# Kernel tuning notes

Hardware: AMD Instinct MI355X
Metric: run time of the kernel (lower is better)

The kernel has to match this reference:

```python
import jax, jax.numpy as jnp
import numpy as np
import math

HIDDEN = 1024
HEADS = 16
HEAD_DIM = HIDDEN // HEADS


def setup_inputs() -> dict:
    key = jax.random.key(0)
    ks = jax.random.split(key, 9)
    s = 1.0 / math.sqrt(HIDDEN)
    return {
        "x": jax.random.normal(ks[0], (4, 2048, HIDDEN), dtype=jnp.float32),
        "Wq": jax.random.normal(ks[1], (HIDDEN, HIDDEN), dtype=jnp.float32) * s,
        "bq": jnp.zeros((HIDDEN,), dtype=jnp.float32),
        "Wk": jax.random.normal(ks[2], (HIDDEN, HIDDEN), dtype=jnp.float32) * s,
        "bk": jnp.zeros((HIDDEN,), dtype=jnp.float32),
        "Wv": jax.random.normal(ks[3], (HIDDEN, HIDDEN), dtype=jnp.float32) * s,
        "bv": jnp.zeros((HIDDEN,), dtype=jnp.float32),
        "Wo": jax.random.normal(ks[4], (HIDDEN, HIDDEN), dtype=jnp.float32) * s,
        "bo": jnp.zeros((HIDDEN,), dtype=jnp.float32),
    }


def reference(x, Wq, bq, Wk, bk, Wv, bv, Wo, bo):
    B, L, D = x.shape
    H, hd = HEADS, HEAD_DIM
    # QKV projections (weights stored as [in, out], i.e. torch W.T)
    q = (x @ Wq + bq).reshape(B, L, H, hd).transpose(0, 2, 1, 3)  # [B,H,L,hd]
    k = (x @ Wk + bk).reshape(B, L, H, hd).transpose(0, 2, 1, 3)
    v = (x @ Wv + bv).reshape(B, L, H, hd).transpose(0, 2, 1, 3)
    scores = jnp.einsum("bhqd,bhkd->bhqk", q, k) / math.sqrt(hd)  # [B,H,L,L]
    causal_mask = jnp.triu(jnp.full((L, L), -jnp.inf, dtype=scores.dtype), k=1)
    att = jax.nn.softmax(scores + causal_mask, axis=-1)
    out = jnp.einsum("bhqk,bhkd->bhqd", att, v)  # [B,H,L,hd]
    out = out.transpose(0, 2, 1, 3).reshape(B, L, D)
    return out @ Wo + bo
```

## Files before the change

### kernel.cpp

```cpp
#include <hip/hip_runtime.h>
#include <stdint.h>

#define LOG2E 1.44269504088896340736f

typedef __attribute__((ext_vector_type(8))) short short8;
typedef __attribute__((ext_vector_type(4))) float float4v;
typedef __attribute__((ext_vector_type(4))) unsigned int uint4v;
typedef __attribute__((ext_vector_type(2))) unsigned int uint2v;

typedef const __attribute__((address_space(1))) unsigned int gu32;
typedef __attribute__((address_space(3))) unsigned int lu32;

__device__ __forceinline__ void async16(const unsigned short* g, unsigned short* l){
  __builtin_amdgcn_global_load_lds((gu32*)g, (lu32*)l, 16, 0, 0);
}

__device__ __forceinline__ unsigned short f2bf(float f){
  union { float f; unsigned int u; } v; v.f = f;
  unsigned int u = v.u;
  return (unsigned short)((u + 0x7FFFu + ((u >> 16) & 1u)) >> 16);
}
__device__ __forceinline__ unsigned int pkbf(float a, float b){
  unsigned int r;
  asm("v_cvt_pk_bf16_f32 %0, %1, %2" : "=v"(r) : "v"(a), "v"(b));
  return r;
}

__device__ __forceinline__ void pl32(unsigned int &a, unsigned int &b){
#if __has_builtin(__builtin_amdgcn_permlane32_swap)
  uint2v r = __builtin_amdgcn_permlane32_swap(a, b, false, false);
  a = r[0]; b = r[1];
#else
  asm("v_permlane32_swap_b32 %0, %1" : "+v"(a), "+v"(b));
#endif
}
__device__ __forceinline__ void pl16(unsigned int &a, unsigned int &b){
#if __has_builtin(__builtin_amdgcn_permlane16_swap)
  uint2v r = __builtin_amdgcn_permlane16_swap(a, b, false, false);
  a = r[0]; b = r[1];
#else
  asm("v_permlane16_swap_b32 %0, %1" : "+v"(a), "+v"(b));
#endif
}

__global__ void prelude_kernel(const float* __restrict__ x, unsigned short* __restrict__ xb,
                               const float* __restrict__ Wq, const float* __restrict__ Wk,
                               const float* __restrict__ Wv, const float* __restrict__ Wo,
                               unsigned short* __restrict__ wqkvT, unsigned short* __restrict__ woT){
  __shared__ float tileS[64][68];
  const int bid = blockIdx.x;
  if (bid < 4096){
    int t = bid * 256 + threadIdx.x;
    const float4v* xp = (const float4v*)x;
    float4v a = xp[2*t], b = xp[2*t+1];
    short8 o;
    o[0]=(short)f2bf(a[0]); o[1]=(short)f2bf(a[1]); o[2]=(short)f2bf(a[2]); o[3]=(short)f2bf(a[3]);
    o[4]=(short)f2bf(b[0]); o[5]=(short)f2bf(b[1]); o[6]=(short)f2bf(b[2]); o[7]=(short)f2bf(b[3]);
    ((short8*)xb)[t] = o;
    return;
  }
  const int wid = bid - 4096;
  int mat = wid >> 8, tile = wid & 255;
  int tk = tile >> 4, tn = tile & 15;
  const float* W = (mat==0)?Wq:(mat==1)?Wk:(mat==2)?Wv:Wo;
  int k0 = tk*64, n0 = tn*64;
  int tid = threadIdx.x;
  #pragma unroll
  for (int it=0; it<4; ++it){
    int idx = tid + it*256;
    int r = idx >> 4, c4 = idx & 15;
    float4v v = *(const float4v*)&W[(uint64_t)(k0+r)*1024 + n0 + c4*4];
    tileS[r][c4*4+0]=v[0]; tileS[r][c4*4+1]=v[1]; tileS[r][c4*4+2]=v[2]; tileS[r][c4*4+3]=v[3];
  }
  __syncthreads();
  unsigned short* dst; int nbase;
  if (mat<3){ dst = wqkvT; nbase = mat*1024 + n0; } else { dst = woT; nbase = n0; }
  #pragma unroll
  for (int it=0; it<2; ++it){
    int idx = tid + it*256;
    int n = idx >> 3, g = idx & 7;
    short8 o;
    #pragma unroll
    for (int j=0;j<8;++j) o[j] = (short)f2bf(tileS[g*8+j][n]);
    *(short8*)&dst[(uint64_t)(nbase+n)*1024 + k0 + g*8] = o;
  }
}

template<int EPI>
__global__ __launch_bounds__(256, 2) void gemm_kernel(
    const unsigned short* __restrict__ A, const unsigned short* __restrict__ BT,
    const float* __restrict__ bias0, const float* __restrict__ bias1, const float* __restrict__ bias2,
    unsigned short* __restrict__ oq, unsigned short* __restrict__ ok,
    unsigned short* __restrict__ ov, float* __restrict__ of)
{
  __shared__ __attribute__((aligned(16))) unsigned short lS[2*128*64];
  unsigned short* lA = lS;
  unsigned short* lB = lS + 128*64;
  const int tid = threadIdx.x, lane = tid & 63, wave = tid >> 6;
  const int wr = wave >> 1, wc = wave & 1;
  const int by = blockIdx.x & 63, bx = blockIdx.x >> 6;
  const int m0 = by * 128, n0 = bx * 128;
  const int c = lane & 15, quad = lane >> 4;
  const float QSCALE = 0.125f * LOG2E;

  float4v acc[4][4];
  #pragma unroll
  for (int i=0;i<4;++i)
    #pragma unroll
    for (int j=0;j<4;++j) acc[i][j] = (float4v){0.f,0.f,0.f,0.f};

  for (int kt = 0; kt < 16; ++kt){
    __syncthreads();
    #pragma unroll
    for (int it=0; it<4; ++it){
      int gl = (wave*4+it)*64 + lane;
      int row = gl >> 3, gp = gl & 7, gs = gp ^ (row & 7);
      async16(&A[(uint64_t)(m0+row)*1024 + kt*64 + gs*8], &lA[gl*8]);
    }
    #pragma unroll
    for (int it=0; it<4; ++it){
      int gl = (wave*4+it)*64 + lane;
      int row = gl >> 3, gp = gl & 7, gs = gp ^ (row & 7);
      async16(&BT[(uint64_t)(n0+row)*1024 + kt*64 + gs*8], &lB[gl*8]);
    }
    __syncthreads();
    #pragma unroll
    for (int kk=0; kk<2; ++kk){
      short8 af[4], bf[4];
      #pragma unroll
      for (int i=0;i<4;++i){
        int row = wr*64 + i*16 + c;
        int g = (quad + kk*4) ^ (row & 7);
        af[i] = *(const short8*)&lA[row*64 + g*8];
      }
      #pragma unroll
      for (int j=0;j<4;++j){
        int row = wc*64 + j*16 + c;
        int g = (quad + kk*4) ^ (row & 7);
        bf[j] = *(const short8*)&lB[row*64 + g*8];
      }
      #pragma unroll
      for (int i=0;i<4;++i)
        #pragma unroll
        for (int j=0;j<4;++j)
          acc[i][j] = __builtin_amdgcn_mfma_f32_16x16x32_bf16(af[i], bf[j], acc[i][j], 0, 0, 0);
    }
  }

  if (EPI == 0){
    const int sel = bx >> 3;
    const int n0l = n0 & 1023;
    const int h0 = n0l >> 6;
    const int bb = m0 >> 11, l0 = m0 & 2047;
    const float* bp = (sel==0)?bias0:(sel==1)?bias1:bias2;
    float bj[4];
    #pragma unroll
    for (int j=0;j<4;++j) bj[j] = bp[n0l + wc*64 + j*16 + c];
    __syncthreads();
    if (sel < 2){
      unsigned short* dst = (sel==0)?oq:ok;
      #pragma unroll
      for (int i=0;i<4;++i){
        #pragma unroll
        for (int r=0;r<4;++r){
          int mloc = wr*64 + i*16 + quad*4 + r;
          #pragma unroll
          for (int j=0;j<4;++j){
            float v = acc[i][j][r] + bj[j];
            if (sel == 0) v *= QSCALE;
            int col = wc*64 + j*16 + c;
            int gg = col >> 3;
            int gs2 = (gg & 8) | ((gg & 7) ^ (mloc & 7));
            lS[mloc*128 + gs2*8 + (col & 7)] = f2bf(v);
          }
        }
      }
      __syncthreads();
      #pragma unroll
      for (int it=0; it<8; ++it){
        int gl = it*256 + tid;
        int row = gl >> 4, gg = gl & 15;
        int gs2 = (gg & 8) | ((gg & 7) ^ (row & 7));
        short8 w = *(const short8*)&lS[row*128 + gs2*8];
        int hh = h0 + (gg >> 3);
        *(short8*)&dst[((uint64_t)(bb*16 + hh)*2048 + l0 + row)*64 + (gg & 7)*8] = w;
      }
    } else {
      #pragma unroll
      for (int i=0;i<4;++i){
        #pragma unroll
        for (int r=0;r<4;++r){
          int mloc = wr*64 + i*16 + quad*4 + r;
          int mgg = mloc >> 3;
          #pragma unroll
          for (int j=0;j<4;++j){
            float v = acc[i][j][r] + bj[j];
            int col = wc*64 + j*16 + c;
            int gsT = (mgg & 8) | ((mgg & 7) ^ (col & 7));
            lS[col*128 + gsT*8 + (mloc & 7)] = f2bf(v);
          }
        }
      }
      __syncthreads();
      #pragma unroll
      for (int it=0; it<8; ++it){
        int idx = it*256 + tid;
        int mg = idx & 15, cc = idx >> 4;
        int gsT2 = (mg & 8) | ((mg & 7) ^ (cc & 7));
        short8 w = *(const short8*)&lS[cc*128 + gsT2*8];
        int hh = h0 + (cc >> 6), d = cc & 63;
        *(short8*)&ov[((uint64_t)(bb*16 + hh)*64 + d)*2048 + l0 + mg*8] = w;
      }
    }
  } else {
    float* lf = (float*)lS;
    float bj[4];
    #pragma unroll
    for (int j=0;j<4;++j) bj[j] = bias0[n0 + wc*64 + j*16 + c];
    #pragma unroll
    for (int half=0; half<2; ++half){
      __syncthreads();
      if (wr == half){
        #pragma unroll
        for (int i=0;i<4;++i){
          #pragma unroll
          for (int r=0;r<4;++r){
            int lrow = i*16 + quad*4 + r;
            #pragma unroll
            for (int j=0;j<4;++j){
              int col = wc*64 + j*16 + c;
              int gg = col >> 2;
              int gs2 = (gg & 24) | ((gg & 7) ^ (lrow & 7));
              lf[lrow*128 + gs2*4 + (col & 3)] = acc[i][j][r] + bj[j];
            }
          }
        }
      }
      __syncthreads();
      #pragma unroll
      for (int it=0; it<8; ++it){
        int gl = it*256 + tid;
        int lrow = gl >> 5, gg = gl & 31;
        int gs2 = (gg & 24) | ((gg & 7) ^ (lrow & 7));
        float4v w = *(const float4v*)&lf[lrow*128 + gs2*4];
        *(float4v*)&of[(uint64_t)(m0 + half*64 + lrow)*1024 + n0 + gg*4] = w;
      }
    }
  }
}

__global__ __launch_bounds__(256, 3) void attn_kernel(
    const unsigned short* __restrict__ q, const unsigned short* __restrict__ k,
    const unsigned short* __restrict__ vt, unsigned short* __restrict__ o)
{
  __shared__ __attribute__((aligned(16))) unsigned short lK[2][64*64];
  __shared__ __attribute__((aligned(16))) unsigned short lV[2][64*64];

  const int idx = blockIdx.x;
  const int bh = idx & 63;
  const int g4 = idx >> 8;
  const int u4 = (idx >> 6) & 3;
  const int qt = (g4==0) ? (15 - u4) : (g4==1) ? (8 + u4) : (g4==2) ? (7 - u4) : u4;
  const int tid = threadIdx.x, lane = tid & 63, wave = tid >> 6;
  const int c = lane & 15, quad = lane >> 4;

  const unsigned short* qh = q  + (uint64_t)bh * (2048*64);
  const unsigned short* kh = k  + (uint64_t)bh * (2048*64);
  const unsigned short* vh = vt + (uint64_t)bh * (64*2048);

  short8 qf[2][2];
  #pragma unroll
  for (int u=0;u<2;++u)
    #pragma unroll
    for (int kk=0;kk<2;++kk){
      int row = qt*128 + u*64 + wave*16 + c;
      qf[u][kk] = *(const short8*)&qh[(uint64_t)row*64 + (kk*4+quad)*8];
    }

  #pragma unroll
  for (int it=0; it<2; ++it){
    int gl = (wave*2+it)*64 + lane;
    int row = gl >> 3, gp = gl & 7, gs = gp ^ (row & 7);
    async16(&kh[(uint64_t)row*64 + gs*8], &lK[0][gl*8]);
    async16(&vh[(uint64_t)row*2048 + gs*8], &lV[0][gl*8]);
  }

  const float4v z4 = {0.f,0.f,0.f,0.f};
  const uint4v onesu = {0x3F803F80u,0x3F803F80u,0x3F803F80u,0x3F803F80u};
  const short8 ones8 = __builtin_bit_cast(short8, onesu);

  float4v accO[2][4];
  #pragma unroll
  for (int u=0;u<2;++u)
    #pragma unroll
    for (int t=0;t<4;++t) accO[u][t] = z4;
  float4v accL4[2];
  accL4[0] = z4; accL4[1] = z4;

  const int ktEnd = 2*qt + 1;

  for (int kt = 0; kt <= ktEnd; ++kt){
    __syncthreads();
    const int cb = kt & 1;

    if (kt < ktEnd){
      const int nb = 1 - cb;
      #pragma unroll
      for (int it=0; it<2; ++it){
        int gl = (wave*2+it)*64 + lane;
        int row = gl >> 3, gp = gl & 7, gs = gp ^ (row & 7);
        async16(&kh[(uint64_t)((kt+1)*64 + row)*64 + gs*8], &lK[nb][gl*8]);
        async16(&vh[(uint64_t)row*2048 + (kt+1)*64 + gs*8], &lV[nb][gl*8]);
      }
    }

    const bool doU0  = (kt != ktEnd);
    const bool lastT = (kt == ktEnd);
    const bool diag0 = doU0 && (kt == 2*qt);

    float4v s[2][4];
    #pragma unroll
    for (int kk=0; kk<2; ++kk){
      short8 kf[4];
      #pragma unroll
      for (int j=0;j<4;++j){
        if (lastT && j > wave) continue;
        int row = j*16 + c;
        int g = (kk*4 + quad) ^ (row & 7);
        kf[j] = *(const short8*)&lK[cb][row*64 + g*8];
      }
      #pragma unroll
      for (int j=0;j<4;++j){
        if (lastT && j > wave) continue;
        s[1][j] = __builtin_amdgcn_mfma_f32_16x16x32_bf16(kf[j], qf[1][kk],
                    (kk==0)? z4 : s[1][j], 0, 0, 0);
      }
      if (doU0){
        #pragma unroll
        for (int j=0;j<4;++j){
          if (diag0 && j > wave) continue;
          s[0][j] = __builtin_amdgcn_mfma_f32_16x16x32_bf16(kf[j], qf[0][kk],
                      (kk==0)? z4 : s[0][j], 0, 0, 0);
        }
      }
    }

    short8 pa[2][2];
    #pragma unroll
    for (int u=1;u>=0;--u){
      if (u==0 && !doU0) continue;
      const bool isDiagU = (u==1) ? lastT : diag0;
      const int qb_u = qt*128 + u*64 + wave*16;
      const bool needMask = (kt*64 + 63 > qb_u);
      const int qg = qb_u + c;
      unsigned int w[4][2];
      #pragma unroll
      for (int j=0;j<4;++j){
        if (isDiagU && j > wave){ w[j][0]=0u; w[j][1]=0u; continue; }
        float p0,p1,p2,p3;
        {
          float4v sv = s[u][j];
          p0 = __builtin_amdgcn_exp2f(sv[0]);
          p1 = __builtin_amdgcn_exp2f(sv[1]);
          p2 = __builtin_amdgcn_exp2f(sv[2]);
          p3 = __builtin_amdgcn_exp2f(sv[3]);
        }
        if (needMask){
          int keyb = kt*64 + j*16 + quad*4;
          if (keyb + 0 > qg) p0 = 0.f;
          if (keyb + 1 > qg) p1 = 0.f;
          if (keyb + 2 > qg) p2 = 0.f;
          if (keyb + 3 > qg) p3 = 0.f;
        }
        w[j][0] = pkbf(p0,p1);
        w[j][1] = pkbf(p2,p3);
      }
      #pragma unroll
      for (int kk=0;kk<2;++kk){
        if (isDiagU && kk==1 && wave < 2) continue;
        unsigned int a0 = w[2*kk+0][0], b0 = w[2*kk+1][0];
        unsigned int a1 = w[2*kk+0][1], b1 = w[2*kk+1][1];
        pl32(a0,b0); pl32(a1,b1);
        pl16(a0,b0); pl16(a1,b1);
        uint4v uv; uv[0]=a0; uv[1]=a1; uv[2]=b0; uv[3]=b1;
        pa[u][kk] = __builtin_bit_cast(short8, uv);
      }
    }

    #pragma unroll
    for (int kk=0; kk<2; ++kk){
      const bool needU1 = !(lastT && kk==1 && wave < 2);
      const bool needU0 = doU0 && !(diag0 && kk==1 && wave < 2);
      short8 bv[4];
      if (needU1 || needU0){
        #pragma unroll
        for (int t=0;t<4;++t){
          int row = t*16 + c;
          int g = (kk*4 + quad) ^ (row & 7);
          bv[t] = *(const short8*)&lV[cb][row*64 + g*8];
        }
      }
      if (needU1){
        #pragma unroll
        for (int t=0;t<4;++t)
          accO[1][t] = __builtin_amdgcn_mfma_f32_16x16x32_bf16(pa[1][kk], bv[t], accO[1][t], 0, 0, 0);
        accL4[1] = __builtin_amdgcn_mfma_f32_16x16x32_bf16(pa[1][kk], ones8, accL4[1], 0, 0, 0);
      }
      if (needU0){
        #pragma unroll
        for (int t=0;t<4;++t)
          accO[0][t] = __builtin_amdgcn_mfma_f32_16x16x32_bf16(pa[0][kk], bv[t], accO[0][t], 0, 0, 0);
        accL4[0] = __builtin_amdgcn_mfma_f32_16x16x32_bf16(pa[0][kk], ones8, accL4[0], 0, 0, 0);
      }
    }
  }

  __syncthreads();

  const int b = bh >> 4, h = bh & 15;
  unsigned short* lPf = &lK[0][0];
  #pragma unroll
  for (int u=0;u<2;++u){
    #pragma unroll
    for (int r=0;r<4;++r){
      float rinv = 1.0f / accL4[u][r];
      int mloc = u*64 + wave*16 + quad*4 + r;
      #pragma unroll
      for (int t=0;t<4;++t){
        int col = t*16 + c;
        int gg = col >> 3;
        int gs2 = gg ^ (mloc & 7);
        lPf[mloc*64 + gs2*8 + (col & 7)] = f2bf(accO[u][t][r] * rinv);
      }
    }
  }
  __syncthreads();
  #pragma unroll
  for (int it=0; it<4; ++it){
    int gl = it*256 + tid;
    int row = gl >> 3, gg = gl & 7;
    int gs2 = gg ^ (row & 7);
    short8 w = *(const short8*)&lPf[row*64 + gs2*8];
    uint64_t m = (uint64_t)b*2048 + qt*128 + row;
    *(short8*)&o[m*1024 + h*64 + gg*8] = w;
  }
}

extern "C" void kernel_launch(void* const* d_in, const int* in_sizes, int n_in,
                              void* d_out, int out_size, void* d_ws, size_t ws_size,
                              hipStream_t stream)
{
  (void)in_sizes; (void)n_in; (void)out_size; (void)ws_size;
  const float* x  = (const float*)d_in[0];
  const float* Wq = (const float*)d_in[1];
  const float* bq = (const float*)d_in[2];
  const float* Wk = (const float*)d_in[3];
  const float* bk = (const float*)d_in[4];
  const float* Wv = (const float*)d_in[5];
  const float* bv = (const float*)d_in[6];
  const float* Wo = (const float*)d_in[7];
  const float* bo = (const float*)d_in[8];
  float* out = (float*)d_out;

  char* ws = (char*)d_ws;
  unsigned short* xb    = (unsigned short*)(ws);
  unsigned short* wqkvT = (unsigned short*)(ws + (16ull<<20));
  unsigned short* woT   = (unsigned short*)(ws + (22ull<<20));
  unsigned short* qb    = (unsigned short*)(ws + (24ull<<20));
  unsigned short* kb    = (unsigned short*)(ws + (40ull<<20));
  unsigned short* vtb   = (unsigned short*)(ws + (56ull<<20));
  unsigned short* ab    = xb;

  prelude_kernel<<<5120, 256, 0, stream>>>(x, xb, Wq, Wk, Wv, Wo, wqkvT, woT);
  gemm_kernel<0><<<1536, 256, 0, stream>>>(xb, wqkvT, bq, bk, bv, qb, kb, vtb, nullptr);
  attn_kernel<<<1024, 256, 0, stream>>>(qb, kb, vtb, ab);
  gemm_kernel<1><<<512, 256, 0, stream>>>(ab, woT, bo, nullptr, nullptr, nullptr, nullptr, nullptr, out);
}
```

Measured before the change: 239.3 us.

## Use 256x256-tile double-buffered QKV GEMM with grouped block mapping

Splits the templated GEMM into a dedicated QKV kernel and an output-projection kernel. The QKV kernel now uses 512-thread blocks computing 256x256 tiles, which cuts global reloads of A and B per output element. It issues async global-to-LDS loads two stages ahead with vmcnt waits, so loads overlap with MFMA work. Block IDs are remapped so neighbouring blocks are spread across groups of 8, aiming for better cache locality. The cost is 128KB of LDS and 384 blocks, which lowers occupancy and may leave some CUs idle at the tail.

Measured after the change: 241.9 us. About the same (+1.1%).

```diff
diff --git a/kernel.cpp b/kernel.cpp
--- a/kernel.cpp
+++ b/kernel.cpp
@@ -86,12 +86,166 @@
   }
 }
 
-template<int EPI>
-__global__ __launch_bounds__(256, 2) void gemm_kernel(
+__global__ __launch_bounds__(512, 2) void gemm_qkv_kernel(
     const unsigned short* __restrict__ A, const unsigned short* __restrict__ BT,
     const float* __restrict__ bias0, const float* __restrict__ bias1, const float* __restrict__ bias2,
     unsigned short* __restrict__ oq, unsigned short* __restrict__ ok,
-    unsigned short* __restrict__ ov, float* __restrict__ of)
+    unsigned short* __restrict__ ov)
+{
+  __shared__ __attribute__((aligned(16))) unsigned short lsAll[65536];
+  const int tid = threadIdx.x, lane = tid & 63, wave = tid >> 6;
+  const int wr = wave >> 2, wc = wave & 3;
+  const int id = blockIdx.x;
+  const int wgid = (id & 7) * 48 + (id >> 3);
+  const int by = wgid & 31, bx = wgid >> 5;
+  const int m0 = by * 256, n0 = bx * 256;
+  const int c = lane & 15, quad = lane >> 4;
+  const float QSCALE = 0.125f * LOG2E;
+
+  float4v acc[8][4];
+  #pragma unroll
+  for (int i=0;i<8;++i)
+    #pragma unroll
+    for (int j=0;j<4;++j) acc[i][j] = (float4v){0.f,0.f,0.f,0.f};
+
+  auto STAGE = [&](int kt2, int bufc){
+    #pragma unroll
+    for (int l=0;l<4;++l){
+      int gl = l*512 + tid;
+      int row = gl >> 3, gp = gl & 7, gs = gp ^ (row & 7);
+      async16(&A[(uint64_t)(m0+row)*1024 + kt2*64 + gs*8], &lsAll[bufc*16384 + gl*8]);
+    }
+    #pragma unroll
+    for (int l=0;l<4;++l){
+      int gl = l*512 + tid;
+      int row = gl >> 3, gp = gl & 7, gs = gp ^ (row & 7);
+      async16(&BT[(uint64_t)(n0+row)*1024 + kt2*64 + gs*8], &lsAll[32768 + bufc*16384 + gl*8]);
+    }
+  };
+
+  STAGE(0, 0);
+  STAGE(1, 1);
+  asm volatile("s_waitcnt vmcnt(8)" ::: "memory");
+  __builtin_amdgcn_s_barrier();
+
+  for (int kt = 0; kt < 16; ++kt){
+    const int cur = kt & 1;
+    const unsigned short* lA = &lsAll[cur*16384];
+    const unsigned short* lB = &lsAll[32768 + cur*16384];
+    #pragma unroll
+    for (int kk=0; kk<2; ++kk){
+      short8 bf[4], af[4];
+      #pragma unroll
+      for (int j=0;j<4;++j){
+        int row = wc*64 + j*16 + c;
+        int g = (kk*4 + quad) ^ (row & 7);
+        bf[j] = *(const short8*)&lB[row*64 + g*8];
+      }
+      #pragma unroll
+      for (int i4=0;i4<4;++i4){
+        int row = wr*128 + i4*16 + c;
+        int g = (kk*4 + quad) ^ (row & 7);
+        af[i4] = *(const short8*)&lA[row*64 + g*8];
+      }
+      #pragma unroll
+      for (int i4=0;i4<4;++i4)
+        #pragma unroll
+        for (int j=0;j<4;++j)
+          acc[i4][j] = __builtin_amdgcn_mfma_f32_16x16x32_bf16(af[i4], bf[j], acc[i4][j], 0, 0, 0);
+      #pragma unroll
+      for (int i4=0;i4<4;++i4){
+        int row = wr*128 + 64 + i4*16 + c;
+        int g = (kk*4 + quad) ^ (row & 7);
+        af[i4] = *(const short8*)&lA[row*64 + g*8];
+      }
+      #pragma unroll
+      for (int i4=0;i4<4;++i4)
+        #pragma unroll
+        for (int j=0;j<4;++j)
+          acc[4+i4][j] = __builtin_amdgcn_mfma_f32_16x16x32_bf16(af[i4], bf[j], acc[4+i4][j], 0, 0, 0);
+    }
+    if (kt < 15){
+      __builtin_amdgcn_s_barrier();
+      if (kt < 14){
+        STAGE(kt+2, cur);
+        asm volatile("s_waitcnt vmcnt(8)" ::: "memory");
+      } else {
+        asm volatile("s_waitcnt vmcnt(0)" ::: "memory");
+      }
+      __builtin_amdgcn_s_barrier();
+    }
+  }
+
+  const int sel = bx >> 2;
+  const int n0l = (bx & 3) * 256;
+  const int h0 = n0l >> 6;
+  const int bb = m0 >> 11, l0 = m0 & 2047;
+  const float* bp = (sel==0)?bias0:(sel==1)?bias1:bias2;
+  float bj[4];
+  #pragma unroll
+  for (int j=0;j<4;++j) bj[j] = bp[n0l + wc*64 + j*16 + c];
+  __syncthreads();
+  unsigned short* lE = lsAll;
+  if (sel < 2){
+    unsigned short* dst = (sel==0)?oq:ok;
+    #pragma unroll
+    for (int i=0;i<8;++i){
+      #pragma unroll
+      for (int r=0;r<4;++r){
+        int row = wr*128 + i*16 + quad*4 + r;
+        #pragma unroll
+        for (int j=0;j<4;++j){
+          float v = acc[i][j][r] + bj[j];
+          if (sel == 0) v *= QSCALE;
+          int col = wc*64 + j*16 + c;
+          int gg = col >> 3;
+          int gsw = (gg & 24) | ((gg & 7) ^ (row & 7));
+          lE[row*256 + gsw*8 + (col & 7)] = f2bf(v);
+        }
+      }
+    }
+    __syncthreads();
+    #pragma unroll
+    for (int it=0; it<16; ++it){
+      int gl = it*512 + tid;
+      int row = gl >> 5, gg = gl & 31;
+      int gsw = (gg & 24) | ((gg & 7) ^ (row & 7));
+      short8 w = *(const short8*)&lE[row*256 + gsw*8];
+      int hh = h0 + (gg >> 3);
+      *(short8*)&dst[((uint64_t)(bb*16 + hh)*2048 + l0 + row)*64 + (gg & 7)*8] = w;
+    }
+  } else {
+    #pragma unroll
+    for (int i=0;i<8;++i){
+      #pragma unroll
+      for (int r=0;r<4;++r){
+        int mloc = wr*128 + i*16 + quad*4 + r;
+        int mgg = mloc >> 3;
+        #pragma unroll
+        for (int j=0;j<4;++j){
+          float v = acc[i][j][r] + bj[j];
+          int col = wc*64 + j*16 + c;
+          int gsT = (mgg & 24) | ((mgg & 7) ^ (col & 7));
+          lE[col*256 + gsT*8 + (mloc & 7)] = f2bf(v);
+        }
+      }
+    }
+    __syncthreads();
+    #pragma unroll
+    for (int it=0; it<16; ++it){
+      int idx = it*512 + tid;
+      int mg = idx & 31, cc = idx >> 5;
+      int gsT2 = (mg & 24) | ((mg & 7) ^ (cc & 7));
+      short8 w = *(const short8*)&lE[cc*256 + gsT2*8];
+      int hh = h0 + (cc >> 6), d = cc & 63;
+      *(short8*)&ov[((uint64_t)(bb*16 + hh)*64 + d)*2048 + l0 + mg*8] = w;
+    }
+  }
+}
+
+__global__ __launch_bounds__(256, 2) void gemm_out_kernel(
+    const unsigned short* __restrict__ A, const unsigned short* __restrict__ BT,
+    const float* __restrict__ bias0, float* __restrict__ of)
 {
   __shared__ __attribute__((aligned(16))) unsigned short lS[2*128*64];
   unsigned short* lA = lS;
@@ -101,7 +255,6 @@
   const int by = blockIdx.x & 63, bx = blockIdx.x >> 6;
   const int m0 = by * 128, n0 = bx * 128;
   const int c = lane & 15, quad = lane >> 4;
-  const float QSCALE = 0.125f * LOG2E;
 
   float4v acc[4][4];
   #pragma unroll
@@ -147,104 +300,37 @@
     }
   }
 
-  if (EPI == 0){
-    const int sel = bx >> 3;
-    const int n0l = n0 & 1023;
-    const int h0 = n0l >> 6;
-    const int bb = m0 >> 11, l0 = m0 & 2047;
-    const float* bp = (sel==0)?bias0:(sel==1)?bias1:bias2;
-    float bj[4];
-    #pragma unroll
-    for (int j=0;j<4;++j) bj[j] = bp[n0l + wc*64 + j*16 + c];
-    __syncthreads();
-    if (sel < 2){
-      unsigned short* dst = (sel==0)?oq:ok;
+  float* lf = (float*)lS;
+  float bj[4];
+  #pragma unroll
+  for (int j=0;j<4;++j) bj[j] = bias0[n0 + wc*64 + j*16 + c];
+  #pragma unroll
+  for (int half=0; half<2; ++half){
+    __syncthreads();
+    if (wr == half){
       #pragma unroll
       for (int i=0;i<4;++i){
         #pragma unroll
         for (int r=0;r<4;++r){
-          int mloc = wr*64 + i*16 + quad*4 + r;
+          int lrow = i*16 + quad*4 + r;
           #pragma unroll
           for (int j=0;j<4;++j){
-            float v = acc[i][j][r] + bj[j];
-            if (sel == 0) v *= QSCALE;
             int col = wc*64 + j*16 + c;
-            int gg = col >> 3;
-            int gs2 = (gg & 8) | ((gg & 7) ^ (mloc & 7));
-            lS[mloc*128 + gs2*8 + (col & 7)] = f2bf(v);
+            int gg = col >> 2;
+            int gs2 = (gg & 24) | ((gg & 7) ^ (lrow & 7));
+            lf[lrow*128 + gs2*4 + (col & 3)] = acc[i][j][r] + bj[j];
           }
         }
       }
-      __syncthreads();
-      #pragma unroll
-      for (int it=0; it<8; ++it){
-        int gl = it*256 + tid;
-        int row = gl >> 4, gg = gl & 15;
-        int gs2 = (gg & 8) | ((gg & 7) ^ (row & 7));
-        short8 w = *(const short8*)&lS[row*128 + gs2*8];
-        int hh = h0 + (gg >> 3);
-        *(short8*)&dst[((uint64_t)(bb*16 + hh)*2048 + l0 + row)*64 + (gg & 7)*8] = w;
-      }
-    } else {
-      #pragma unroll
-      for (int i=0;i<4;++i){
-        #pragma unroll
-        for (int r=0;r<4;++r){
-          int mloc = wr*64 + i*16 + quad*4 + r;
-          int mgg = mloc >> 3;
-          #pragma unroll
-          for (int j=0;j<4;++j){
-            float v = acc[i][j][r] + bj[j];
-            int col = wc*64 + j*16 + c;
-            int gsT = (mgg & 8) | ((mgg & 7) ^ (col & 7));
-            lS[col*128 + gsT*8 + (mloc & 7)] = f2bf(v);
-          }
-        }
-      }
-      __syncthreads();
-      #pragma unroll
-      for (int it=0; it<8; ++it){
-        int idx = it*256 + tid;
-        int mg = idx & 15, cc = idx >> 4;
-        int gsT2 = (mg & 8) | ((mg & 7) ^ (cc & 7));
-        short8 w = *(const short8*)&lS[cc*128 + gsT2*8];
-        int hh = h0 + (cc >> 6), d = cc & 63;
-        *(short8*)&ov[((uint64_t)(bb*16 + hh)*64 + d)*2048 + l0 + mg*8] = w;
-      }
-    }
-  } else {
-    float* lf = (float*)lS;
-    float bj[4];
-    #pragma unroll
-    for (int j=0;j<4;++j) bj[j] = bias0[n0 + wc*64 + j*16 + c];
-    #pragma unroll
-    for (int half=0; half<2; ++half){
-      __syncthreads();
-      if (wr == half){
-        #pragma unroll
-        for (int i=0;i<4;++i){
-          #pragma unroll
-          for (int r=0;r<4;++r){
-            int lrow = i*16 + quad*4 + r;
-            #pragma unroll
-            for (int j=0;j<4;++j){
-              int col = wc*64 + j*16 + c;
-              int gg = col >> 2;
-              int gs2 = (gg & 24) | ((gg & 7) ^ (lrow & 7));
-              lf[lrow*128 + gs2*4 + (col & 3)] = acc[i][j][r] + bj[j];
-            }
-          }
-        }
-      }
-      __syncthreads();
-      #pragma unroll
-      for (int it=0; it<8; ++it){
-        int gl = it*256 + tid;
-        int lrow = gl >> 5, gg = gl & 31;
-        int gs2 = (gg & 24) | ((gg & 7) ^ (lrow & 7));
-        float4v w = *(const float4v*)&lf[lrow*128 + gs2*4];
-        *(float4v*)&of[(uint64_t)(m0 + half*64 + lrow)*1024 + n0 + gg*4] = w;
-      }
+    }
+    __syncthreads();
+    #pragma unroll
+    for (int it=0; it<8; ++it){
+      int gl = it*256 + tid;
+      int lrow = gl >> 5, gg = gl & 31;
+      int gs2 = (gg & 24) | ((gg & 7) ^ (lrow & 7));
+      float4v w = *(const float4v*)&lf[lrow*128 + gs2*4];
+      *(float4v*)&of[(uint64_t)(m0 + half*64 + lrow)*1024 + n0 + gg*4] = w;
     }
   }
 }
@@ -472,7 +558,7 @@
   unsigned short* ab    = xb;
 
   prelude_kernel<<<5120, 256, 0, stream>>>(x, xb, Wq, Wk, Wv, Wo, wqkvT, woT);
-  gemm_kernel<0><<<1536, 256, 0, stream>>>(xb, wqkvT, bq, bk, bv, qb, kb, vtb, nullptr);
+  gemm_qkv_kernel<<<384, 512, 0, stream>>>(xb, wqkvT, bq, bk, bv, qb, kb, vtb);
   attn_kernel<<<1024, 256, 0, stream>>>(qb, kb, vtb, ab);
-  gemm_kernel<1><<<512, 256, 0, stream>>>(ab, woT, bo, nullptr, nullptr, nullptr, nullptr, nullptr, out);
-}
+  gemm_out_kernel<<<512, 256, 0, stream>>>(ab, woT, bo, out);
+}
```
